# Performance work log

Measured on AMD Instinct MI355X. Metric: run time of the kernel, lower is better.

## Reference

```python
import jax, jax.numpy as jnp
import numpy as np
from jax import lax

BITS_P = 8   # parameter fake-quant bits
BITS_A = 8   # activation fake-quant bits
D_STATE = 16
DT_RANK = 2
EPS = 1e-5


def fake_quant(t, bits):
    """Min-max fake quantization (forward math of QuantizationFunction)."""
    mn, mx = t.min(), t.max()
    step = (mx - mn) / (2 ** bits - 1)
    step_safe = jnp.where(step == 0, 1.0, step)
    q = jnp.round((jnp.clip(t, mn, mx) - mn) / step_safe) * step_safe + mn
    return jnp.where(step == 0, t, q)


def quant_ste(t, bits):
    # straight-through estimator (backward returns grad unchanged)
    return t + lax.stop_gradient(fake_quant(t, bits) - t)


def layernorm(x, g, b):
    mu = x.mean(-1, keepdims=True)
    var = ((x - mu) ** 2).mean(-1, keepdims=True)
    return (x - mu) * lax.rsqrt(var + EPS) * g + b


def mamba_block(x4d, ln_g, ln_b, W_in, conv_w, conv_b, W_xproj, W_dt, dt_bias, A_log, D_ssm, W_out):
    B, M, H, W = x4d.shape
    L = H * W
    di = W_in.shape[1] // 2  # d_inner = 2*M
    seq = x4d.reshape(B, M, L).transpose(0, 2, 1)          # [B,L,M]
    h = layernorm(seq, ln_g, ln_b)
    xz = h @ W_in                                           # [B,L,2*di]
    xs, z = xz[..., :di], xz[..., di:]
    # causal depthwise conv1d, kernel 4
    xc = xs.transpose(0, 2, 1)                              # [B,di,L]
    xc = lax.conv_general_dilated(xc, conv_w[:, None, :], (1,), ((3, 0),),
                                  dimension_numbers=('NCH', 'OIH', 'NCH'),
                                  feature_group_count=di)
    xc = jax.nn.silu(xc + conv_b[None, :, None]).transpose(0, 2, 1)  # [B,L,di]
    dbl = xc @ W_xproj                                      # [B,L,dt_rank+2*ds]
    dt_r = dbl[..., :DT_RANK]
    Bm = dbl[..., DT_RANK:DT_RANK + D_STATE]                # [B,L,ds]
    Cm = dbl[..., DT_RANK + D_STATE:]                       # [B,L,ds]
    dt = jax.nn.softplus(dt_r @ W_dt + dt_bias)             # [B,L,di]
    A = -jnp.exp(A_log)                                     # [di,ds]

    def step(hprev, inp):
        dt_t, B_t, C_t, x_t = inp                           # [B,di],[B,ds],[B,ds],[B,di]
        dA = jnp.exp(dt_t[..., None] * A)                   # [B,di,ds]
        hn = hprev * dA + (dt_t * x_t)[..., None] * B_t[:, None, :]
        y = jnp.einsum('bds,bs->bd', hn, C_t)
        return hn, y

    h0 = jnp.zeros((B, di, D_STATE), x4d.dtype)
    _, ys = lax.scan(step, h0, (dt.transpose(1, 0, 2), Bm.transpose(1, 0, 2),
                                Cm.transpose(1, 0, 2), xc.transpose(1, 0, 2)))
    ys = ys.transpose(1, 0, 2)                              # [B,L,di]
    ys = (ys + xc * D_ssm) * jax.nn.silu(z)
    out = ys @ W_out                                        # [B,L,M]
    seq = seq + out                                         # residual
    return seq.transpose(0, 2, 1).reshape(B, M, H, W)


def reference(x, stem_w, bn_gamma, bn_beta, bn_mean, bn_var,
              ln_g, ln_b, W_in, conv_w, conv_b, W_xproj, W_dt, dt_bias,
              A_log, D_ssm, W_out, proj_w, fc_w, fc_b):
    B = x.shape[0]
    # stem: fake-quant conv -> BN (eval stats) -> SiLU
    w_q = quant_ste(stem_w, BITS_P)
    h = lax.conv_general_dilated(x, w_q, (2, 2), ((1, 1), (1, 1)),
                                 dimension_numbers=('NCHW', 'OIHW', 'NCHW'))
    h = (h - bn_mean[None, :, None, None]) * lax.rsqrt(bn_var + EPS)[None, :, None, None]
    h = h * bn_gamma[None, :, None, None] + bn_beta[None, :, None, None]
    h = jax.nn.silu(h)                                      # [B,32,16,16]
    for i in range(ln_g.shape[0]):
        h = mamba_block(h, ln_g[i], ln_b[i], W_in[i], conv_w[i], conv_b[i],
                        W_xproj[i], W_dt[i], dt_bias[i], A_log[i], D_ssm[i], W_out[i])
    # fake-quant 1x1 conv head + fc
    pw = quant_ste(proj_w, BITS_P)
    h = lax.conv_general_dilated(h, pw, (1, 1), ((0, 0), (0, 0)),
                                 dimension_numbers=('NCHW', 'OIHW', 'NCHW'))
    h = h.reshape(B, -1)                                    # [B,2048]
    fw = quant_ste(fc_w, BITS_P)
    h = h @ fw.T + fc_b                                     # [B,512]
    h = jax.nn.sigmoid(h)
    return quant_ste(h, BITS_A)


def setup_inputs() -> dict:
    key = jax.random.key(0)
    ks = jax.random.split(key, 20)
    B, M, di, nl = 2048, 32, 64, 2
    s = 0.05
    inp = {
        'x': jax.random.normal(ks[0], (B, 2, 32, 32), jnp.float32),
        'stem_w': jax.random.normal(ks[1], (M, 2, 3, 3), jnp.float32) * 0.2,
        'bn_gamma': jnp.ones((M,), jnp.float32),
        'bn_beta': jnp.zeros((M,), jnp.float32),
        'bn_mean': jax.random.normal(ks[2], (M,), jnp.float32) * 0.1,
        'bn_var': jax.random.uniform(ks[3], (M,), jnp.float32, 0.5, 1.5),
        'ln_g': jnp.ones((nl, M), jnp.float32),
        'ln_b': jnp.zeros((nl, M), jnp.float32),
        'W_in': jax.random.normal(ks[4], (nl, M, 2 * di), jnp.float32) * s,
        'conv_w': jax.random.normal(ks[5], (nl, di, 4), jnp.float32) * 0.2,
        'conv_b': jnp.zeros((nl, di), jnp.float32),
        'W_xproj': jax.random.normal(ks[6], (nl, di, DT_RANK + 2 * D_STATE), jnp.float32) * s,
        'W_dt': jax.random.normal(ks[7], (nl, DT_RANK, di), jnp.float32) * s,
        'dt_bias': jax.random.normal(ks[8], (nl, di), jnp.float32) * 0.1,
        'A_log': jnp.log(jnp.tile(jnp.arange(1.0, D_STATE + 1.0), (nl, di, 1))).astype(jnp.float32),
        'D_ssm': jnp.ones((nl, di), jnp.float32),
        'W_out': jax.random.normal(ks[9], (nl, di, M), jnp.float32) * s,
        'proj_w': jax.random.normal(ks[10], (8, M, 1, 1), jnp.float32) * 0.1,
        'fc_w': jax.random.normal(ks[11], (512, 8 * 16 * 16), jnp.float32) * 0.02,
        'fc_b': jnp.zeros((512,), jnp.float32),
    }
    return inp
```

## Files before the change

kernel.cpp:

```cpp
#include <hip/hip_runtime.h>
#include <hip/hip_fp16.h>
#include <math.h>

#define NB   2048
#define M_   32
#define L_   256
#define DI   64
#define DS_  16
#define EPSF 1e-5f

__device__ __forceinline__ float sigmf(float x){ return 1.0f/(1.0f+__expf(-x)); }
__device__ __forceinline__ float siluf(float x){ return x*sigmf(x); }
__device__ __forceinline__ float softplusf(float x){
  return fmaxf(x,0.0f) + log1pf(__expf(-fabsf(x)));
}

__device__ __forceinline__ void blk_minmax(float& mn, float& mx){
  for (int off = 32; off >= 1; off >>= 1){
    mn = fminf(mn, __shfl_down(mn, off, 64));
    mx = fmaxf(mx, __shfl_down(mx, off, 64));
  }
  __shared__ float smn[4], smx[4];
  int w = threadIdx.x >> 6;
  if ((threadIdx.x & 63) == 0){ smn[w] = mn; smx[w] = mx; }
  __syncthreads();
  if (threadIdx.x == 0){
    int nw = (int)(blockDim.x >> 6);
    for (int i = 1; i < nw; ++i){ mn = fminf(mn, smn[i]); mx = fmaxf(mx, smx[i]); }
  }
}

__global__ void k_minmax_part(const float* __restrict__ t, int n, float* __restrict__ part){
  float mn = 3.402823466e38f, mx = -3.402823466e38f;
  for (int i = blockIdx.x*blockDim.x + threadIdx.x; i < n; i += gridDim.x*blockDim.x){
    float v = t[i]; mn = fminf(mn, v); mx = fmaxf(mx, v);
  }
  blk_minmax(mn, mx);
  if (threadIdx.x == 0){ part[blockIdx.x*2] = mn; part[blockIdx.x*2+1] = mx; }
}

__global__ void k_minmax_final(const float* __restrict__ part, int nparts, float* __restrict__ qp){
  float mn = 3.402823466e38f, mx = -3.402823466e38f;
  for (int i = threadIdx.x; i < nparts; i += blockDim.x){
    mn = fminf(mn, part[i*2]); mx = fmaxf(mx, part[i*2+1]);
  }
  blk_minmax(mn, mx);
  if (threadIdx.x == 0){
    qp[0] = mn; qp[1] = mx; qp[2] = (mx - mn) / 255.0f;
  }
}

__global__ void k_quant(const float* __restrict__ t, float* __restrict__ q, int n,
                        const float* __restrict__ qp){
  float mn = qp[0], mx = qp[1], step = qp[2];
  bool zero = (step == 0.0f);
  for (int i = blockIdx.x*blockDim.x + threadIdx.x; i < n; i += gridDim.x*blockDim.x){
    float v = t[i];
    float c = fminf(fmaxf(v, mn), mx);
    float r = rintf((c - mn) / (zero ? 1.0f : step));
    float o = fmaf(r, step, mn);
    q[i] = zero ? v : o;
  }
}

__launch_bounds__(256)
__global__ void k_stem(const float* __restrict__ x, const float* __restrict__ wq,
                       const float* __restrict__ bn_g, const float* __restrict__ bn_b,
                       const float* __restrict__ bn_m, const float* __restrict__ bn_v,
                       __half* __restrict__ h){
  int b = blockIdx.x;
  __shared__ float xs[2048];
  const float* xb = x + (size_t)b*2048;
  for (int i = threadIdx.x; i < 2048; i += 256) xs[i] = xb[i];
  __syncthreads();
  int l = threadIdx.x;
  int oy = l >> 4, ox = l & 15;
  for (int m = 0; m < M_; ++m){
    float acc = 0.f;
    #pragma unroll
    for (int c = 0; c < 2; ++c){
      #pragma unroll
      for (int ky = 0; ky < 3; ++ky){
        int iy = oy*2 - 1 + ky;
        if (iy < 0 || iy >= 32) continue;
        #pragma unroll
        for (int kx = 0; kx < 3; ++kx){
          int ix = ox*2 - 1 + kx;
          if (ix < 0 || ix >= 32) continue;
          acc = fmaf(xs[c*1024 + iy*32 + ix], wq[((m*2 + c)*3 + ky)*3 + kx], acc);
        }
      }
    }
    float r = (acc - bn_m[m]) * rsqrtf(bn_v[m] + EPSF) * bn_g[m] + bn_b[m];
    h[((size_t)b*M_ + m)*L_ + l] = __float2half(siluf(r));
  }
}

__launch_bounds__(256)
__global__ void k_a(const __half* __restrict__ h, const float* __restrict__ lng,
                    const float* __restrict__ lnb, const float* __restrict__ W_in,
                    const float* __restrict__ conv_w, const float* __restrict__ conv_b,
                    __half* __restrict__ xc){
  const int b = blockIdx.x, l = threadIdx.x;
  __shared__ __half2 xsb[L_][33];
  const __half* hb = h + (size_t)b*M_*L_;
  float hnreg[M_];
  {
    float s = 0.f;
    #pragma unroll
    for (int m = 0; m < M_; ++m){ hnreg[m] = __half2float(hb[m*L_ + l]); s += hnreg[m]; }
    float mu = s * (1.0f/32.0f);
    float v = 0.f;
    #pragma unroll
    for (int m = 0; m < M_; ++m){ float dd = hnreg[m]-mu; v += dd*dd; }
    float rs = rsqrtf(v*(1.0f/32.0f) + EPSF);
    #pragma unroll
    for (int m = 0; m < M_; ++m) hnreg[m] = (hnreg[m]-mu)*rs*lng[m] + lnb[m];
  }
  {
    float acc[DI];
    #pragma unroll
    for (int d = 0; d < DI; ++d) acc[d] = 0.f;
    #pragma unroll
    for (int m = 0; m < M_; ++m){
      float hv = hnreg[m];
      const float* wr = W_in + m*128;
      #pragma unroll
      for (int d = 0; d < DI; ++d) acc[d] = fmaf(hv, wr[d], acc[d]);
    }
    #pragma unroll
    for (int q = 0; q < 32; ++q) xsb[l][q] = __floats2half2_rn(acc[2*q], acc[2*q+1]);
  }
  __syncthreads();
  {
    __half2* xcrow = (__half2*)(xc + ((size_t)b*L_ + l)*DI);
    const int r3 = l-3, r2 = l-2, r1 = l-1;
    #pragma unroll
    for (int q = 0; q < 32; ++q){
      float2 a0 = (r3 >= 0) ? __half22float2(xsb[r3][q]) : make_float2(0.f,0.f);
      float2 a1 = (r2 >= 0) ? __half22float2(xsb[r2][q]) : make_float2(0.f,0.f);
      float2 a2 = (r1 >= 0) ? __half22float2(xsb[r1][q]) : make_float2(0.f,0.f);
      float2 a3 = __half22float2(xsb[l][q]);
      int d0 = 2*q, d1 = 2*q+1;
      float s0 = fmaf(conv_w[d0*4+0],a0.x, fmaf(conv_w[d0*4+1],a1.x,
                 fmaf(conv_w[d0*4+2],a2.x, fmaf(conv_w[d0*4+3],a3.x, conv_b[d0]))));
      float s1 = fmaf(conv_w[d1*4+0],a0.y, fmaf(conv_w[d1*4+1],a1.y,
                 fmaf(conv_w[d1*4+2],a2.y, fmaf(conv_w[d1*4+3],a3.y, conv_b[d1]))));
      xcrow[q] = __floats2half2_rn(siluf(s0), siluf(s1));
    }
  }
}

__launch_bounds__(256)
__global__ void k_b(const __half* __restrict__ xc, const float* __restrict__ W_xproj,
                    __half* __restrict__ bc){
  const int b = blockIdx.x, l = threadIdx.x;
  const __half2* xrow = (const __half2*)(xc + ((size_t)b*L_ + l)*DI);
  float acc[34];
  #pragma unroll
  for (int j = 0; j < 34; ++j) acc[j] = 0.f;
  #pragma unroll
  for (int q = 0; q < 32; ++q){
    float2 xv = __half22float2(xrow[q]);
    const float* w0 = W_xproj + (2*q)*34;
    const float* w1 = w0 + 34;
    #pragma unroll
    for (int j = 0; j < 34; ++j)
      acc[j] = fmaf(xv.x, w0[j], fmaf(xv.y, w1[j], acc[j]));
  }
  __half2* w2 = (__half2*)(bc + ((size_t)b*L_ + l)*40);
  #pragma unroll
  for (int q = 0; q < 8; ++q) w2[q]   = __floats2half2_rn(acc[2+2*q],  acc[3+2*q]);
  #pragma unroll
  for (int q = 0; q < 8; ++q) w2[8+q] = __floats2half2_rn(acc[18+2*q], acc[19+2*q]);
  w2[16] = __floats2half2_rn(acc[0], acc[1]);
}

__attribute__((amdgpu_waves_per_eu(1)))
__launch_bounds__(64)
__global__ void k_scan(__half* __restrict__ xc, const __half* __restrict__ bc,
                       const float* __restrict__ W_dt, const float* __restrict__ dt_bias,
                       const float* __restrict__ A_log, const float* __restrict__ D_ssm){
  const int b = blockIdx.x, d = threadIdx.x;
  __shared__ float4 bcs4[320];
  __shared__ float4 xcs4[512];
  const __half* bcsh = (const __half*)bcs4;
  const __half* xcs  = (const __half*)xcs4;
  const float LOG2E = 1.44269504088896340736f;
  const float wdt0 = W_dt[d], wdt1 = W_dt[64+d], dtb = dt_bias[d], Dd = D_ssm[d];
  float hst[DS_];
  #pragma unroll
  for (int s = 0; s < DS_; ++s) hst[s] = 0.f;
  const float a0 = -__expf(A_log[d*DS_]) * LOG2E;
  bool ok = true;
  #pragma unroll
  for (int s = 1; s < DS_; ++s){
    float as = -__expf(A_log[d*DS_ + s]) * LOG2E;
    ok = ok && (fabsf(as - (float)(s+1)*a0) <= 1e-4f*fabsf(as));
  }
  const bool fast = (__all((int)ok) != 0);
  if (fast){
    const float4* gb = (const float4*)(bc + (size_t)b*L_*40);
    const float4* gx = (const float4*)(xc + (size_t)b*L_*DI);
    __half* xout = xc + (size_t)b*L_*DI + d;
    for (int c = 0; c < 4; ++c){
      __syncthreads();
      #pragma unroll
      for (int k = 0; k < 5; ++k) bcs4[k*64 + d] = gb[c*320 + k*64 + d];
      #pragma unroll
      for (int k = 0; k < 8; ++k) xcs4[k*64 + d] = gx[c*512 + k*64 + d];
      __syncthreads();
      for (int i = 0; i < 64; ++i){
        const __half2* row2 = (const __half2*)(bcsh + i*40);
        float2 dtp = __half22float2(row2[16]);
        float tt = fmaf(dtp.x, wdt0, fmaf(dtp.y, wdt1, dtb));
        float e  = __expf(-fabsf(tt));
        float dtv = fmaxf(tt, 0.f) + __logf(1.f + e);
        float xv = __half2float(xcs[i*DI + d]);
        float dtx = dtv * xv;
        float r1 = exp2f(dtv * a0);
        float r2 = r1*r1, r3 = r2*r1, r4 = r2*r2;
        float r5 = r4*r1, r6 = r4*r2, r7 = r4*r3, r8 = r4*r4;
        float dA[16] = {r1,r2,r3,r4,r5,r6,r7,r8,
                        r8*r1,r8*r2,r8*r3,r8*r4,r8*r5,r8*r6,r8*r7,r8*r8};
        float yp = 0.f;
        #pragma unroll
        for (int s2 = 0; s2 < 8; ++s2){
          float2 Bp = __half22float2(row2[s2]);
          float2 Cp = __half22float2(row2[8+s2]);
          hst[2*s2]   = fmaf(hst[2*s2],   dA[2*s2],   dtx*Bp.x);
          yp = fmaf(hst[2*s2],   Cp.x, yp);
          hst[2*s2+1] = fmaf(hst[2*s2+1], dA[2*s2+1], dtx*Bp.y);
          yp = fmaf(hst[2*s2+1], Cp.y, yp);
        }
        xout[(size_t)(c*64 + i)*DI] = __float2half(fmaf(xv, Dd, yp));
      }
    }
  } else {
    float A2r[DS_];
    #pragma unroll
    for (int s = 0; s < DS_; ++s) A2r[s] = -__expf(A_log[d*DS_ + s]) * LOG2E;
    const __half* rowg = bc + (size_t)b*L_*40;
    __half* xpg = xc + (size_t)b*L_*DI + d;
    for (int ll = 0; ll < L_; ++ll){
      float xv = __half2float(*xpg);
      float t0 = __half2float(rowg[32]), t1 = __half2float(rowg[33]);
      float tt = fmaf(t0, wdt0, fmaf(t1, wdt1, dtb));
      float e  = __expf(-fabsf(tt));
      float dtv = fmaxf(tt, 0.f) + __logf(1.f + e);
      float dtx = dtv * xv;
      float yp = 0.f;
      #pragma unroll
      for (int s = 0; s < DS_; ++s){
        float dA = exp2f(dtv * A2r[s]);
        hst[s] = fmaf(hst[s], dA, dtx * __half2float(rowg[s]));
        yp = fmaf(hst[s], __half2float(rowg[16+s]), yp);
      }
      *xpg = __float2half(fmaf(xv, Dd, yp));
      rowg += 40; xpg += DI;
    }
  }
}

__launch_bounds__(256)
__global__ void k_c(const __half* __restrict__ xc, const float* __restrict__ lng,
                    const float* __restrict__ lnb, const float* __restrict__ W_in,
                    const float* __restrict__ W_out, __half* __restrict__ h){
  const int b = blockIdx.x, l = threadIdx.x;
  __half* hb = h + (size_t)b*M_*L_;
  float hnreg[M_], hraw[M_];
  {
    float s = 0.f;
    #pragma unroll
    for (int m = 0; m < M_; ++m){ hraw[m] = __half2float(hb[m*L_ + l]); s += hraw[m]; }
    float mu = s * (1.0f/32.0f);
    float v = 0.f;
    #pragma unroll
    for (int m = 0; m < M_; ++m){ float dd = hraw[m]-mu; v += dd*dd; }
    float rs = rsqrtf(v*(1.0f/32.0f) + EPSF);
    #pragma unroll
    for (int m = 0; m < M_; ++m) hnreg[m] = (hraw[m]-mu)*rs*lng[m] + lnb[m];
  }
  const __half2* yrow = (const __half2*)(xc + ((size_t)b*L_ + l)*DI);
  float accm[M_];
  #pragma unroll
  for (int m = 0; m < M_; ++m) accm[m] = 0.f;
  #pragma unroll
  for (int c2 = 0; c2 < 2; ++c2){
    float z[32];
    #pragma unroll
    for (int j = 0; j < 32; ++j) z[j] = 0.f;
    #pragma unroll
    for (int m = 0; m < M_; ++m){
      float hv = hnreg[m];
      const float* wr = W_in + m*128 + 64 + c2*32;
      #pragma unroll
      for (int j = 0; j < 32; ++j) z[j] = fmaf(hv, wr[j], z[j]);
    }
    #pragma unroll
    for (int j2 = 0; j2 < 16; ++j2){
      float2 yv = __half22float2(yrow[c2*16 + j2]);
      float g0 = yv.x * siluf(z[2*j2]);
      float g1 = yv.y * siluf(z[2*j2+1]);
      const float* w0 = W_out + (c2*32 + 2*j2)*32;
      const float* w1 = w0 + 32;
      #pragma unroll
      for (int m = 0; m < M_; ++m)
        accm[m] = fmaf(g0, w0[m], fmaf(g1, w1[m], accm[m]));
    }
  }
  #pragma unroll
  for (int m = 0; m < M_; ++m)
    hb[m*L_ + l] = __float2half(hraw[m] + accm[m]);
}

__launch_bounds__(256)
__global__ void k_proj(const __half* __restrict__ h, const float* __restrict__ pw,
                       float* __restrict__ h2){
  int b = blockIdx.x;
  __shared__ float hsd[M_*L_];
  for (int i = threadIdx.x; i < M_*L_; i += 256)
    hsd[i] = __half2float(h[(size_t)b*M_*L_ + i]);
  __syncthreads();
  int l = threadIdx.x;
  #pragma unroll
  for (int c = 0; c < 8; ++c){
    float acc = 0.f;
    #pragma unroll
    for (int m = 0; m < M_; ++m) acc = fmaf(hsd[m*L_ + l], pw[c*M_ + m], acc);
    h2[(size_t)b*2048 + c*L_ + l] = acc;
  }
}

__launch_bounds__(256)
__global__ void k_fc(const float* __restrict__ A, const float* __restrict__ W,
                     const float* __restrict__ bias, float* __restrict__ out){
  int bi = blockIdx.x, bj = blockIdx.y;
  __shared__ float As[32][68];
  __shared__ float Ws[32][68];
  int tid = threadIdx.x;
  int ti = tid >> 4, tj = tid & 15;
  float acc[4][4];
  #pragma unroll
  for (int u=0;u<4;++u){
    #pragma unroll
    for (int v=0;v<4;++v) acc[u][v]=0.f;
  }
  for (int k0 = 0; k0 < 2048; k0 += 32){
    __syncthreads();
    #pragma unroll
    for (int r8 = 0; r8 < 8; ++r8){
      int i = tid + r8*256;
      int r = i >> 5, c = i & 31;
      As[c][r] = A[(size_t)(bi*64+r)*2048 + k0 + c];
      Ws[c][r] = W[(size_t)(bj*64+r)*2048 + k0 + c];
    }
    __syncthreads();
    #pragma unroll
    for (int k = 0; k < 32; ++k){
      float4 av = *(const float4*)&As[k][ti*4];
      float4 wv = *(const float4*)&Ws[k][tj*4];
      float a4[4] = {av.x,av.y,av.z,av.w};
      float w4[4] = {wv.x,wv.y,wv.z,wv.w};
      #pragma unroll
      for (int u=0;u<4;++u){
        #pragma unroll
        for (int v=0;v<4;++v) acc[u][v] = fmaf(a4[u], w4[v], acc[u][v]);
      }
    }
  }
  #pragma unroll
  for (int u=0;u<4;++u){
    int r = bi*64 + ti*4 + u;
    #pragma unroll
    for (int v=0;v<4;++v){
      int c = bj*64 + tj*4 + v;
      out[(size_t)r*512 + c] = sigmf(acc[u][v] + bias[c]);
    }
  }
}

static const size_t OF_H    = 0;
static const size_t OF_XC   = 8388608;
static const size_t OF_BC   = 25165824;
static const size_t OF_H2   = 35651584;
static const size_t OF_LG   = 39845888;
static const size_t OF_WQF  = 40894464;
static const size_t OF_WQS  = 41943040;
static const size_t OF_WQP  = 41944064;
static const size_t OF_PART = 41944576;
static const size_t OF_QP   = 41945088;
static const size_t WS_FLOATS_NEEDED = 41945104;

extern "C" void kernel_launch(void* const* d_in, const int* in_sizes, int n_in,
                              void* d_out, int out_size, void* d_ws, size_t ws_size,
                              hipStream_t stream){
  (void)in_sizes; (void)n_in; (void)out_size;
  if (ws_size < WS_FLOATS_NEEDED * sizeof(float)) return;
  const float* x      = (const float*)d_in[0];
  const float* stem_w = (const float*)d_in[1];
  const float* bn_g   = (const float*)d_in[2];
  const float* bn_b   = (const float*)d_in[3];
  const float* bn_m   = (const float*)d_in[4];
  const float* bn_v   = (const float*)d_in[5];
  const float* ln_g   = (const float*)d_in[6];
  const float* ln_b   = (const float*)d_in[7];
  const float* W_in   = (const float*)d_in[8];
  const float* conv_w = (const float*)d_in[9];
  const float* conv_b = (const float*)d_in[10];
  const float* W_xp   = (const float*)d_in[11];
  const float* W_dt   = (const float*)d_in[12];
  const float* dt_b   = (const float*)d_in[13];
  const float* A_log  = (const float*)d_in[14];
  const float* D_ssm  = (const float*)d_in[15];
  const float* W_out  = (const float*)d_in[16];
  const float* proj_w = (const float*)d_in[17];
  const float* fc_w   = (const float*)d_in[18];
  const float* fc_b   = (const float*)d_in[19];
  float* ws   = (float*)d_ws;
  __half* bh  = (__half*)(ws + OF_H);
  __half* bxc = (__half*)(ws + OF_XC);
  __half* bbc = (__half*)(ws + OF_BC);
  float* bh2  = ws + OF_H2;
  float* blg  = ws + OF_LG;
  float* wqf  = ws + OF_WQF;
  float* wqs  = ws + OF_WQS;
  float* wqp  = ws + OF_WQP;
  float* part = ws + OF_PART;
  float* qp   = ws + OF_QP;

  k_minmax_part<<<1,256,0,stream>>>(stem_w, 576, part);
  k_minmax_final<<<1,256,0,stream>>>(part, 1, qp+0);
  k_quant<<<3,256,0,stream>>>(stem_w, wqs, 576, qp+0);

  k_minmax_part<<<1,256,0,stream>>>(proj_w, 256, part);
  k_minmax_final<<<1,256,0,stream>>>(part, 1, qp+4);
  k_quant<<<1,256,0,stream>>>(proj_w, wqp, 256, qp+4);

  k_minmax_part<<<256,256,0,stream>>>(fc_w, 1048576, part);
  k_minmax_final<<<1,256,0,stream>>>(part, 256, qp+8);
  k_quant<<<1024,256,0,stream>>>(fc_w, wqf, 1048576, qp+8);

  k_stem<<<NB,256,0,stream>>>(x, wqs, bn_g, bn_b, bn_m, bn_v, bh);

  for (int i = 0; i < 2; ++i){
    k_a<<<NB,256,0,stream>>>(bh, ln_g+i*32, ln_b+i*32, W_in+i*4096,
                             conv_w+i*256, conv_b+i*64, bxc);
    k_b<<<NB,256,0,stream>>>(bxc, W_xp+i*2176, bbc);
    k_scan<<<NB,64,0,stream>>>(bxc, bbc, W_dt+i*128, dt_b+i*64,
                               A_log+i*1024, D_ssm+i*64);
    k_c<<<NB,256,0,stream>>>(bxc, ln_g+i*32, ln_b+i*32, W_in+i*4096,
                             W_out+i*2048, bh);
  }

  k_proj<<<NB,256,0,stream>>>(bh, wqp, bh2);
  dim3 fcg(32, 8);
  k_fc<<<fcg,256,0,stream>>>(bh2, wqf, fc_b, blg);

  k_minmax_part<<<256,256,0,stream>>>(blg, 1048576, part);
  k_minmax_final<<<1,256,0,stream>>>(part, 256, qp+12);
  k_quant<<<1024,256,0,stream>>>(blg, (float*)d_out, 1048576, qp+12);
}
```

Measured before the change: 1.005 ms.

## Fuse x-projection into conv kernel and vectorize scan shared-memory reads

```diff
diff --git a/kernel.cpp b/kernel.cpp
--- a/kernel.cpp
+++ b/kernel.cpp
@@ -97,10 +97,11 @@
 }
 
 __launch_bounds__(256)
-__global__ void k_a(const __half* __restrict__ h, const float* __restrict__ lng,
-                    const float* __restrict__ lnb, const float* __restrict__ W_in,
-                    const float* __restrict__ conv_w, const float* __restrict__ conv_b,
-                    __half* __restrict__ xc){
+__global__ void k_ab(const __half* __restrict__ h, const float* __restrict__ lng,
+                     const float* __restrict__ lnb, const float* __restrict__ W_in,
+                     const float* __restrict__ conv_w, const float* __restrict__ conv_b,
+                     const float* __restrict__ W_xproj,
+                     __half* __restrict__ xc, __half* __restrict__ bc){
   const int b = blockIdx.x, l = threadIdx.x;
   __shared__ __half2 xsb[L_][33];
   const __half* hb = h + (size_t)b*M_*L_;
@@ -132,6 +133,7 @@
     for (int q = 0; q < 32; ++q) xsb[l][q] = __floats2half2_rn(acc[2*q], acc[2*q+1]);
   }
   __syncthreads();
+  float xcv[DI];
   {
     __half2* xcrow = (__half2*)(xc + ((size_t)b*L_ + l)*DI);
     const int r3 = l-3, r2 = l-2, r1 = l-1;
@@ -146,34 +148,29 @@
                  fmaf(conv_w[d0*4+2],a2.x, fmaf(conv_w[d0*4+3],a3.x, conv_b[d0]))));
       float s1 = fmaf(conv_w[d1*4+0],a0.y, fmaf(conv_w[d1*4+1],a1.y,
                  fmaf(conv_w[d1*4+2],a2.y, fmaf(conv_w[d1*4+3],a3.y, conv_b[d1]))));
-      xcrow[q] = __floats2half2_rn(siluf(s0), siluf(s1));
-    }
-  }
-}
-
-__launch_bounds__(256)
-__global__ void k_b(const __half* __restrict__ xc, const float* __restrict__ W_xproj,
-                    __half* __restrict__ bc){
-  const int b = blockIdx.x, l = threadIdx.x;
-  const __half2* xrow = (const __half2*)(xc + ((size_t)b*L_ + l)*DI);
-  float acc[34];
-  #pragma unroll
-  for (int j = 0; j < 34; ++j) acc[j] = 0.f;
-  #pragma unroll
-  for (int q = 0; q < 32; ++q){
-    float2 xv = __half22float2(xrow[q]);
-    const float* w0 = W_xproj + (2*q)*34;
-    const float* w1 = w0 + 34;
-    #pragma unroll
-    for (int j = 0; j < 34; ++j)
-      acc[j] = fmaf(xv.x, w0[j], fmaf(xv.y, w1[j], acc[j]));
-  }
-  __half2* w2 = (__half2*)(bc + ((size_t)b*L_ + l)*40);
-  #pragma unroll
-  for (int q = 0; q < 8; ++q) w2[q]   = __floats2half2_rn(acc[2+2*q],  acc[3+2*q]);
-  #pragma unroll
-  for (int q = 0; q < 8; ++q) w2[8+q] = __floats2half2_rn(acc[18+2*q], acc[19+2*q]);
-  w2[16] = __floats2half2_rn(acc[0], acc[1]);
+      xcv[d0] = siluf(s0);
+      xcv[d1] = siluf(s1);
+      xcrow[q] = __floats2half2_rn(xcv[d0], xcv[d1]);
+    }
+  }
+  {
+    float acc[34];
+    #pragma unroll
+    for (int j = 0; j < 34; ++j) acc[j] = 0.f;
+    #pragma unroll
+    for (int dd = 0; dd < DI; ++dd){
+      float xv = xcv[dd];
+      const float* wr = W_xproj + dd*34;
+      #pragma unroll
+      for (int j = 0; j < 34; ++j) acc[j] = fmaf(xv, wr[j], acc[j]);
+    }
+    __half2* w2 = (__half2*)(bc + ((size_t)b*L_ + l)*40);
+    #pragma unroll
+    for (int q = 0; q < 8; ++q) w2[q]   = __floats2half2_rn(acc[2+2*q],  acc[3+2*q]);
+    #pragma unroll
+    for (int q = 0; q < 8; ++q) w2[8+q] = __floats2half2_rn(acc[18+2*q], acc[19+2*q]);
+    w2[16] = __floats2half2_rn(acc[0], acc[1]);
+  }
 }
 
 __attribute__((amdgpu_waves_per_eu(1)))
@@ -184,7 +181,6 @@
   const int b = blockIdx.x, d = threadIdx.x;
   __shared__ float4 bcs4[320];
   __shared__ float4 xcs4[512];
-  const __half* bcsh = (const __half*)bcs4;
   const __half* xcs  = (const __half*)xcs4;
   const float LOG2E = 1.44269504088896340736f;
   const float wdt0 = W_dt[d], wdt1 = W_dt[64+d], dtb = dt_bias[d], Dd = D_ssm[d];
@@ -210,9 +206,12 @@
       #pragma unroll
       for (int k = 0; k < 8; ++k) xcs4[k*64 + d] = gx[c*512 + k*64 + d];
       __syncthreads();
+      #pragma unroll 2
       for (int i = 0; i < 64; ++i){
-        const __half2* row2 = (const __half2*)(bcsh + i*40);
-        float2 dtp = __half22float2(row2[16]);
+        const float4* rowq = bcs4 + i*5;
+        float4 f0 = rowq[0], f1 = rowq[1], f2 = rowq[2], f3 = rowq[3];
+        __half2 dt2 = ((const __half2*)rowq)[16];
+        float2 dtp = __half22float2(dt2);
         float tt = fmaf(dtp.x, wdt0, fmaf(dtp.y, wdt1, dtb));
         float e  = __expf(-fabsf(tt));
         float dtv = fmaxf(tt, 0.f) + __logf(1.f + e);
@@ -223,16 +222,28 @@
         float r5 = r4*r1, r6 = r4*r2, r7 = r4*r3, r8 = r4*r4;
         float dA[16] = {r1,r2,r3,r4,r5,r6,r7,r8,
                         r8*r1,r8*r2,r8*r3,r8*r4,r8*r5,r8*r6,r8*r7,r8*r8};
-        float yp = 0.f;
+        const __half2* bh0 = (const __half2*)&f0;
+        const __half2* bh1 = (const __half2*)&f1;
+        const __half2* ch0 = (const __half2*)&f2;
+        const __half2* ch1 = (const __half2*)&f3;
+        float yp0=0.f, yp1=0.f, yp2=0.f, yp3=0.f;
         #pragma unroll
-        for (int s2 = 0; s2 < 8; ++s2){
-          float2 Bp = __half22float2(row2[s2]);
-          float2 Cp = __half22float2(row2[8+s2]);
-          hst[2*s2]   = fmaf(hst[2*s2],   dA[2*s2],   dtx*Bp.x);
-          yp = fmaf(hst[2*s2],   Cp.x, yp);
-          hst[2*s2+1] = fmaf(hst[2*s2+1], dA[2*s2+1], dtx*Bp.y);
-          yp = fmaf(hst[2*s2+1], Cp.y, yp);
+        for (int q = 0; q < 4; ++q){
+          float2 Bq = __half22float2(bh0[q]);
+          float2 Cq = __half22float2(ch0[q]);
+          int s = 2*q;
+          hst[s]   = fmaf(hst[s],   dA[s],   dtx*Bq.x);  yp0 = fmaf(hst[s],   Cq.x, yp0);
+          hst[s+1] = fmaf(hst[s+1], dA[s+1], dtx*Bq.y);  yp1 = fmaf(hst[s+1], Cq.y, yp1);
         }
+        #pragma unroll
+        for (int q = 0; q < 4; ++q){
+          float2 Bq = __half22float2(bh1[q]);
+          float2 Cq = __half22float2(ch1[q]);
+          int s = 8 + 2*q;
+          hst[s]   = fmaf(hst[s],   dA[s],   dtx*Bq.x);  yp2 = fmaf(hst[s],   Cq.x, yp2);
+          hst[s+1] = fmaf(hst[s+1], dA[s+1], dtx*Bq.y);  yp3 = fmaf(hst[s+1], Cq.y, yp3);
+        }
+        float yp = (yp0+yp1)+(yp2+yp3);
         xout[(size_t)(c*64 + i)*DI] = __float2half(fmaf(xv, Dd, yp));
       }
     }
@@ -444,9 +455,8 @@
   k_stem<<<NB,256,0,stream>>>(x, wqs, bn_g, bn_b, bn_m, bn_v, bh);
 
   for (int i = 0; i < 2; ++i){
-    k_a<<<NB,256,0,stream>>>(bh, ln_g+i*32, ln_b+i*32, W_in+i*4096,
-                             conv_w+i*256, conv_b+i*64, bxc);
-    k_b<<<NB,256,0,stream>>>(bxc, W_xp+i*2176, bbc);
+    k_ab<<<NB,256,0,stream>>>(bh, ln_g+i*32, ln_b+i*32, W_in+i*4096,
+                              conv_w+i*256, conv_b+i*64, W_xp+i*2176, bxc, bbc);
     k_scan<<<NB,64,0,stream>>>(bxc, bbc, W_dt+i*128, dt_b+i*64,
                                A_log+i*1024, D_ssm+i*64);
     k_c<<<NB,256,0,stream>>>(bxc, ln_g+i*32, ln_b+i*32, W_in+i*4096,
```

Result: faster. 972.4 us (-3.2%).
